# Optimization experiments

Hardware: AMD Instinct MI355X
Metric: run time of the kernel (lower is better)

Reference implementation:

```python
import jax, jax.numpy as jnp
import numpy as np

ALPHA = 0.1  # config['alpha']


def setup_inputs() -> dict:
    key = jax.random.key(0)
    k1, k2, k3, k4, k5 = jax.random.split(key, 5)
    n_bs, bit, n_cls, class_bit, n_train = 128, 48, 100, 16, 10000
    u = jax.random.normal(k1, (n_bs, bit), dtype=jnp.float32)
    # multi-hot labels (float, as in torch: y.float())
    y = jax.random.bernoulli(k2, 0.1, (n_bs, n_cls)).astype(jnp.float32)
    ind = jnp.arange(n_bs, dtype=jnp.int64)  # distinct in-range row indices
    # buffers mid-training: U holds previous class-wise codes, Y previous labels
    U = jax.random.normal(k3, (n_train, n_cls, class_bit), dtype=jnp.float32) * 0.1
    Y = jax.random.bernoulli(k4, 0.1, (n_train, n_cls)).astype(jnp.float32)
    # xavier_uniform-like init for w_D [n_class, bit, class_bit]
    limit = np.sqrt(6.0 / (bit + class_bit)).astype(np.float32)
    w_D = jax.random.uniform(k5, (n_cls, bit, class_bit), dtype=jnp.float32,
                             minval=-limit, maxval=limit)
    return {"u": u, "y": y, "ind": ind, "U": U, "Y": Y, "w_D": w_D}


def reference(u, y, ind, U, Y, w_D):
    # update label buffer: self.Y[ind, :] = y
    Y = Y.at[ind].set(y)
    # u_ = matmul(u, w_D).permute(1,0,2): [n_bs, n_cls, class_bit]
    u_ = jnp.einsum('bk,ckd->bcd', u, w_D)
    # update code buffer with detached u_ (torch: self.U[ind] = u_.data)
    U = U.at[ind].set(jax.lax.stop_gradient(u_))
    # pairwise similarity s: [n_bs, n_train, n_cls]
    s = y[:, None, :] * Y[None, :, :]
    # inner_product: sum over class_bit -> [n_bs, n_train, n_cls]
    ip = jnp.einsum('tcd,bcd->btc', U, u_)
    # stable log(1 + exp(ip)) - s*ip, exactly as the torch expression
    likelihood = (jnp.log1p(jnp.exp(-jnp.abs(ip))) + jnp.maximum(ip, 0.0)
                  - s * ip).mean()
    quantization = ALPHA * jnp.mean((u_ - jnp.sign(u_)) ** 2)
    return likelihood + quantization
```

## Files before the change

kernel.cpp:

```cpp
#include <hip/hip_runtime.h>
#include <math.h>

#define CB 16
#define ALPHA 0.1f
#define LOG2E 1.4426950408889634f
#define LN2F  0.6931471805599453f
#define MAXW 8
#define N_BS 128
#define BIT  48
#define UPAD 52

typedef __bf16 bf16x8 __attribute__((ext_vector_type(8)));
typedef float  f32x16 __attribute__((ext_vector_type(16)));

__global__ __launch_bounds__(256, 4) void loss_fused(
        const float* __restrict__ u, const float* __restrict__ y,
        const float* __restrict__ w_D,
        const float* __restrict__ U, const float* __restrict__ Yb,
        const int* __restrict__ ind,
        float* __restrict__ partials, float* __restrict__ quant_partials,
        int n_cls, int n_train, int ntile, int GY) {
    __shared__ float smf[N_BS * UPAD + 4 * BIT * CB];
    __shared__ int pflag[MAXW * 32];
    float* u_lds   = smf;
    float* wd_lds  = smf + N_BS * UPAD;
    float* u_slice = smf;

    const int tid  = threadIdx.x;
    const int lane = tid & 63;
    const int wid  = tid >> 6;
    const int bx   = blockIdx.x;
    const int by   = blockIdx.y;
    const int c    = bx * 4 + wid;
    const int r    = lane & 31;
    const int h    = lane >> 5;
    const int nw   = (ntile - by + GY - 1) / GY;

    pflag[tid] = -1;
    #pragma unroll
    for (int it = 0; it < N_BS * (BIT / 4) / 256; ++it) {
        int f = it * 256 + tid;
        int b = f / (BIT / 4), k4 = f % (BIT / 4);
        *(float4*)&u_lds[b * UPAD + k4 * 4] =
            *(const float4*)&u[(size_t)b * BIT + k4 * 4];
    }
    #pragma unroll
    for (int it = 0; it < 4 * BIT * (CB / 4) / 256; ++it) {
        int f = it * 256 + tid;
        int cc = f / (BIT * CB / 4), rest = f % (BIT * CB / 4);
        *(float4*)&wd_lds[cc * BIT * CB + rest * 4] =
            *(const float4*)&w_D[(size_t)(bx * 4 + cc) * BIT * CB + rest * 4];
    }
    __syncthreads();

    if (tid < N_BS) {
        int t = ind[tid];
        for (int w = 0; w < nw; ++w) {
            unsigned rl = (unsigned)(t - (by + w * GY) * 32);
            if (rl < 32u) pflag[w * 32 + rl] = tid;
        }
    }

    float acc0[8] = {0,0,0,0,0,0,0,0};
    float acc1[8] = {0,0,0,0,0,0,0,0};
    float acc2[8] = {0,0,0,0,0,0,0,0};
    float acc3[8] = {0,0,0,0,0,0,0,0};
    {
        const float* __restrict__ wdc = wd_lds + wid * BIT * CB + h * 8;
        for (int k4 = 0; k4 < BIT / 4; ++k4) {
            float4 ub0 = *(const float4*)&u_lds[(0 * 32 + r) * UPAD + k4 * 4];
            float4 ub1 = *(const float4*)&u_lds[(1 * 32 + r) * UPAD + k4 * 4];
            float4 ub2 = *(const float4*)&u_lds[(2 * 32 + r) * UPAD + k4 * 4];
            float4 ub3 = *(const float4*)&u_lds[(3 * 32 + r) * UPAD + k4 * 4];
            #pragma unroll
            for (int kk = 0; kk < 4; ++kk) {
                const float* wrow = wdc + (k4 * 4 + kk) * CB;
                float w8[8];
                float4 wa = *(const float4*)(wrow);
                float4 wb = *(const float4*)(wrow + 4);
                w8[0]=wa.x; w8[1]=wa.y; w8[2]=wa.z; w8[3]=wa.w;
                w8[4]=wb.x; w8[5]=wb.y; w8[6]=wb.z; w8[7]=wb.w;
                float s0 = (&ub0.x)[kk], s1 = (&ub1.x)[kk];
                float s2 = (&ub2.x)[kk], s3 = (&ub3.x)[kk];
                #pragma unroll
                for (int j = 0; j < 8; ++j) {
                    acc0[j] = fmaf(s0, w8[j], acc0[j]);
                    acc1[j] = fmaf(s1, w8[j], acc1[j]);
                    acc2[j] = fmaf(s2, w8[j], acc2[j]);
                    acc3[j] = fmaf(s3, w8[j], acc3[j]);
                }
            }
        }
    }

    if (by == 0) {
        float q = 0.f;
        #pragma unroll
        for (int j = 0; j < 8; ++j) {
            float v, sgn, d;
            v = acc0[j]; sgn = (v>0.f)?1.f:((v<0.f)?-1.f:0.f); d = v-sgn; q = fmaf(d,d,q);
            v = acc1[j]; sgn = (v>0.f)?1.f:((v<0.f)?-1.f:0.f); d = v-sgn; q = fmaf(d,d,q);
            v = acc2[j]; sgn = (v>0.f)?1.f:((v<0.f)?-1.f:0.f); d = v-sgn; q = fmaf(d,d,q);
            v = acc3[j]; sgn = (v>0.f)?1.f:((v<0.f)?-1.f:0.f); d = v-sgn; q = fmaf(d,d,q);
        }
        #pragma unroll
        for (int off = 32; off > 0; off >>= 1) q += __shfl_down(q, off, 64);
        if (lane == 0) quant_partials[bx * 4 + wid] = q;
    }

    float ypc0 = y[(size_t)(0 * 32 + r) * n_cls + c];
    float ypc1 = y[(size_t)(1 * 32 + r) * n_cls + c];
    float ypc2 = y[(size_t)(2 * 32 + r) * n_cls + c];
    float ypc3 = y[(size_t)(3 * 32 + r) * n_cls + c];
    float vv[8], ww[8];
    #pragma unroll
    for (int j = 0; j < 8; ++j) {
        ww[j] = acc0[j] + acc1[j] + acc2[j] + acc3[j];
        vv[j] = ypc0*acc0[j] + ypc1*acc1[j] + ypc2*acc2[j] + ypc3*acc3[j];
    }
    #pragma unroll
    for (int m = 1; m < 32; m <<= 1) {
        #pragma unroll
        for (int j = 0; j < 8; ++j) {
            vv[j] += __shfl_xor(vv[j], m, 64);
            ww[j] += __shfl_xor(ww[j], m, 64);
        }
    }

    bf16x8 B0, B1, B2, B3;
    #pragma unroll
    for (int j = 0; j < 8; ++j) {
        B0[j] = (__bf16)(acc0[j] * LOG2E);
        B1[j] = (__bf16)(acc1[j] * LOG2E);
        B2[j] = (__bf16)(acc2[j] * LOG2E);
        B3[j] = (__bf16)(acc3[j] * LOG2E);
    }

    __syncthreads();
    {
        float* dst = u_slice + wid * N_BS * CB + r * CB + h * 8;
        *(float4*)(dst + 0*32*CB)     = make_float4(acc0[0],acc0[1],acc0[2],acc0[3]);
        *(float4*)(dst + 0*32*CB + 4) = make_float4(acc0[4],acc0[5],acc0[6],acc0[7]);
        *(float4*)(dst + 1*32*CB)     = make_float4(acc1[0],acc1[1],acc1[2],acc1[3]);
        *(float4*)(dst + 1*32*CB + 4) = make_float4(acc1[4],acc1[5],acc1[6],acc1[7]);
        *(float4*)(dst + 2*32*CB)     = make_float4(acc2[0],acc2[1],acc2[2],acc2[3]);
        *(float4*)(dst + 2*32*CB + 4) = make_float4(acc2[4],acc2[5],acc2[6],acc2[7]);
        *(float4*)(dst + 3*32*CB)     = make_float4(acc3[0],acc3[1],acc3[2],acc3[3]);
        *(float4*)(dst + 3*32*CB + 4) = make_float4(acc3[4],acc3[5],acc3[6],acc3[7]);
    }
    __syncthreads();

    float acc = 0.f;
    f32x16 zc = {};
    #pragma unroll 1
    for (int w = 0; w < nw; ++w) {
        const int t0  = (by + w * GY) * 32;
        const int row = t0 + r;
        const int rc  = (row < n_train) ? row : (n_train - 1);
        const float* __restrict__ ar = U + ((size_t)rc * n_cls + c) * CB + h * 8;
        float4 a0 = *(const float4*)(ar);
        float4 a1 = *(const float4*)(ar + 4);
        float Yv = Yb[(size_t)rc * n_cls + c];

        const int pf = pflag[w * 32 + r];
        if (pf >= 0) {
            const float* src = u_slice + wid * N_BS * CB + pf * CB + h * 8;
            a0 = *(const float4*)(src);
            a1 = *(const float4*)(src + 4);
            Yv = y[(size_t)pf * n_cls + c];
        }
        if (row >= n_train) {
            a0 = make_float4(0.f, 0.f, 0.f, 0.f); a1 = a0; Yv = 0.f;
        }

        float sv = a0.x*vv[0] + a0.y*vv[1] + a0.z*vv[2] + a0.w*vv[3]
                 + a1.x*vv[4] + a1.y*vv[5] + a1.z*vv[6] + a1.w*vv[7];
        float sw = a0.x*ww[0] + a0.y*ww[1] + a0.z*ww[2] + a0.w*ww[3]
                 + a1.x*ww[4] + a1.y*ww[5] + a1.z*ww[6] + a1.w*ww[7];

        bf16x8 A;
        A[0] = (__bf16)a0.x; A[1] = (__bf16)a0.y;
        A[2] = (__bf16)a0.z; A[3] = (__bf16)a0.w;
        A[4] = (__bf16)a1.x; A[5] = (__bf16)a1.y;
        A[6] = (__bf16)a1.z; A[7] = (__bf16)a1.w;

        float accA = 0.f;
        float pp   = 1.f;
        #pragma unroll
        for (int bt = 0; bt < 4; ++bt) {
            bf16x8 Bf = (bt == 0) ? B0 : (bt == 1) ? B1 : (bt == 2) ? B2 : B3;
            f32x16 D = __builtin_amdgcn_mfma_f32_32x32x16_bf16(A, Bf, zc,
                                                               0, 0, 0);
            float a[16];
            #pragma unroll
            for (int j = 0; j < 16; ++j) {
                float ipa = fabsf(D[j]);
                a[j] = 1.0f + __builtin_amdgcn_exp2f(-ipa);
                accA += ipa;
            }
            #pragma unroll
            for (int s = 1; s < 16; s <<= 1)
                #pragma unroll
                for (int j = 0; j < 16; j += 2 * s) a[j] *= a[j + s];
            pp *= a[0];
        }
        float accL = __builtin_amdgcn_logf(pp);
        acc += LN2F * accL + (0.5f * LN2F) * accA + 0.5f * sw - Yv * sv;
    }

    #pragma unroll
    for (int off = 32; off > 0; off >>= 1)
        acc += __shfl_down(acc, off, 64);
    if (lane == 0) {
        int bid = by * gridDim.x + bx;
        partials[bid * 4 + wid] = acc;
    }
}

__global__ __launch_bounds__(256) void finalize_kernel(
        const float* __restrict__ partials, int nblk,
        const float* __restrict__ quant_partials, int n_quant,
        float* __restrict__ out, double pad_corr,
        double like_scale, double quant_scale) {
    double s = 0.0, q = 0.0;
    for (int i = threadIdx.x; i < nblk; i += 256) s += (double)partials[i];
    for (int i = threadIdx.x; i < n_quant; i += 256) q += (double)quant_partials[i];
    #pragma unroll
    for (int off = 32; off > 0; off >>= 1) {
        s += __shfl_down(s, off, 64);
        q += __shfl_down(q, off, 64);
    }
    __shared__ double dred[4][2];
    int lane = threadIdx.x & 63, wid = threadIdx.x >> 6;
    if (lane == 0) { dred[wid][0] = s; dred[wid][1] = q; }
    __syncthreads();
    if (threadIdx.x == 0) {
        double S = dred[0][0] + dred[1][0] + dred[2][0] + dred[3][0];
        double Q = dred[0][1] + dred[1][1] + dred[2][1] + dred[3][1];
        out[0] = (float)((S - pad_corr) * like_scale + Q * quant_scale);
    }
}

extern "C" void kernel_launch(void* const* d_in, const int* in_sizes, int n_in,
                              void* d_out, int out_size, void* d_ws, size_t ws_size,
                              hipStream_t stream) {
    const float* u   = (const float*)d_in[0];
    const float* y   = (const float*)d_in[1];
    const int*   ind = (const int*)d_in[2];
    const float* U   = (const float*)d_in[3];
    const float* Yb  = (const float*)d_in[4];
    const float* w_D = (const float*)d_in[5];

    const int n_bs    = in_sizes[2];
    const int n_cls   = in_sizes[1] / n_bs;
    const int n_train = in_sizes[4] / n_cls;

    const int totalU = n_bs * n_cls * CB;
    const int ntile  = (n_train + 31) / 32;
    const int GY     = (ntile + MAXW - 1) / MAXW;
    const int gx     = (n_cls + 3) / 4;
    const int nblk   = GY * gx;
    const int npart  = nblk * 4;
    const int nquant = gx * 4;

    char* ws = (char*)d_ws;
    size_t off = 0;
    float* partials = (float*)(ws + off);        off += (size_t)npart * 4;
    float* quant_partials = (float*)(ws + off);  off += (size_t)nquant * 4;

    loss_fused<<<dim3(gx, GY), 256, 0, stream>>>(
        u, y, w_D, U, Yb, ind, partials, quant_partials,
        n_cls, n_train, ntile, GY);

    const double ln2 = 0.6931471805599453;
    const double n_pad = (double)((long long)(ntile * 32 - n_train) *
                                  (long long)n_bs * (long long)n_cls);
    const double pad_corr    = ln2 * n_pad;
    const double like_scale  = 1.0 / ((double)n_bs * n_train * n_cls);
    const double quant_scale = (double)ALPHA / (double)totalU;

    finalize_kernel<<<1, 256, 0, stream>>>(partials, npart,
                                           quant_partials, nquant,
                                           (float*)d_out, pad_corr,
                                           like_scale, quant_scale);
}
```

Before: 49.41 us.

## Drop LDS staging of u and w_D, store u_ slice as packed bf16

The kernel no longer copies u and w_D into shared memory before the small projection matmul. Each lane now reads its operands straight from global memory, relying on caches. The per-wave u_ slice used to patch overwritten buffer rows is stored as packed bf16 pairs in a much smaller LDS array, which also removes one block-wide barrier. This lowers LDS footprint and prologue staging cost, which may help occupancy. In exchange, the prologue does strided, uncoalesced global loads, and the patched rows now enter the fp32 sv/sw dot products at bf16 precision.

New measurement: 58.49 us. +18.4%, slower.

```diff
diff --git a/kernel.cpp b/kernel.cpp
--- a/kernel.cpp
+++ b/kernel.cpp
@@ -8,10 +8,14 @@
 #define MAXW 8
 #define N_BS 128
 #define BIT  48
-#define UPAD 52
 
 typedef __bf16 bf16x8 __attribute__((ext_vector_type(8)));
 typedef float  f32x16 __attribute__((ext_vector_type(16)));
+
+__device__ __forceinline__ unsigned int f2bf(float x) {
+    unsigned int v = __float_as_uint(x);
+    return (v + 0x7FFFu + ((v >> 16) & 1u)) >> 16;
+}
 
 __global__ __launch_bounds__(256, 4) void loss_fused(
         const float* __restrict__ u, const float* __restrict__ y,
@@ -20,11 +24,8 @@
         const int* __restrict__ ind,
         float* __restrict__ partials, float* __restrict__ quant_partials,
         int n_cls, int n_train, int ntile, int GY) {
-    __shared__ float smf[N_BS * UPAD + 4 * BIT * CB];
+    __shared__ unsigned int ubf32[4 * N_BS * 9];
     __shared__ int pflag[MAXW * 32];
-    float* u_lds   = smf;
-    float* wd_lds  = smf + N_BS * UPAD;
-    float* u_slice = smf;
 
     const int tid  = threadIdx.x;
     const int lane = tid & 63;
@@ -37,22 +38,7 @@
     const int nw   = (ntile - by + GY - 1) / GY;
 
     pflag[tid] = -1;
-    #pragma unroll
-    for (int it = 0; it < N_BS * (BIT / 4) / 256; ++it) {
-        int f = it * 256 + tid;
-        int b = f / (BIT / 4), k4 = f % (BIT / 4);
-        *(float4*)&u_lds[b * UPAD + k4 * 4] =
-            *(const float4*)&u[(size_t)b * BIT + k4 * 4];
-    }
-    #pragma unroll
-    for (int it = 0; it < 4 * BIT * (CB / 4) / 256; ++it) {
-        int f = it * 256 + tid;
-        int cc = f / (BIT * CB / 4), rest = f % (BIT * CB / 4);
-        *(float4*)&wd_lds[cc * BIT * CB + rest * 4] =
-            *(const float4*)&w_D[(size_t)(bx * 4 + cc) * BIT * CB + rest * 4];
-    }
     __syncthreads();
-
     if (tid < N_BS) {
         int t = ind[tid];
         for (int w = 0; w < nw; ++w) {
@@ -66,18 +52,22 @@
     float acc2[8] = {0,0,0,0,0,0,0,0};
     float acc3[8] = {0,0,0,0,0,0,0,0};
     {
-        const float* __restrict__ wdc = wd_lds + wid * BIT * CB + h * 8;
+        const float* __restrict__ wdc = w_D + (size_t)c * BIT * CB + h * 8;
+        const float* __restrict__ ub0p = u + (size_t)(0 * 32 + r) * BIT;
+        const float* __restrict__ ub1p = u + (size_t)(1 * 32 + r) * BIT;
+        const float* __restrict__ ub2p = u + (size_t)(2 * 32 + r) * BIT;
+        const float* __restrict__ ub3p = u + (size_t)(3 * 32 + r) * BIT;
         for (int k4 = 0; k4 < BIT / 4; ++k4) {
-            float4 ub0 = *(const float4*)&u_lds[(0 * 32 + r) * UPAD + k4 * 4];
-            float4 ub1 = *(const float4*)&u_lds[(1 * 32 + r) * UPAD + k4 * 4];
-            float4 ub2 = *(const float4*)&u_lds[(2 * 32 + r) * UPAD + k4 * 4];
-            float4 ub3 = *(const float4*)&u_lds[(3 * 32 + r) * UPAD + k4 * 4];
+            float4 ub0 = *(const float4*)(ub0p + k4 * 4);
+            float4 ub1 = *(const float4*)(ub1p + k4 * 4);
+            float4 ub2 = *(const float4*)(ub2p + k4 * 4);
+            float4 ub3 = *(const float4*)(ub3p + k4 * 4);
             #pragma unroll
             for (int kk = 0; kk < 4; ++kk) {
                 const float* wrow = wdc + (k4 * 4 + kk) * CB;
-                float w8[8];
                 float4 wa = *(const float4*)(wrow);
                 float4 wb = *(const float4*)(wrow + 4);
+                float w8[8];
                 w8[0]=wa.x; w8[1]=wa.y; w8[2]=wa.z; w8[3]=wa.w;
                 w8[4]=wb.x; w8[5]=wb.y; w8[6]=wb.z; w8[7]=wb.w;
                 float s0 = (&ub0.x)[kk], s1 = (&ub1.x)[kk];
@@ -127,6 +117,20 @@
         }
     }
 
+    {
+        unsigned int* d0 = &ubf32[(wid * N_BS + 0 * 32 + r) * 9 + h * 4];
+        unsigned int* d1 = &ubf32[(wid * N_BS + 1 * 32 + r) * 9 + h * 4];
+        unsigned int* d2 = &ubf32[(wid * N_BS + 2 * 32 + r) * 9 + h * 4];
+        unsigned int* d3 = &ubf32[(wid * N_BS + 3 * 32 + r) * 9 + h * 4];
+        #pragma unroll
+        for (int j2 = 0; j2 < 4; ++j2) {
+            d0[j2] = f2bf(acc0[2*j2]) | (f2bf(acc0[2*j2+1]) << 16);
+            d1[j2] = f2bf(acc1[2*j2]) | (f2bf(acc1[2*j2+1]) << 16);
+            d2[j2] = f2bf(acc2[2*j2]) | (f2bf(acc2[2*j2+1]) << 16);
+            d3[j2] = f2bf(acc3[2*j2]) | (f2bf(acc3[2*j2+1]) << 16);
+        }
+    }
+
     bf16x8 B0, B1, B2, B3;
     #pragma unroll
     for (int j = 0; j < 8; ++j) {
@@ -136,18 +140,6 @@
         B3[j] = (__bf16)(acc3[j] * LOG2E);
     }
 
-    __syncthreads();
-    {
-        float* dst = u_slice + wid * N_BS * CB + r * CB + h * 8;
-        *(float4*)(dst + 0*32*CB)     = make_float4(acc0[0],acc0[1],acc0[2],acc0[3]);
-        *(float4*)(dst + 0*32*CB + 4) = make_float4(acc0[4],acc0[5],acc0[6],acc0[7]);
-        *(float4*)(dst + 1*32*CB)     = make_float4(acc1[0],acc1[1],acc1[2],acc1[3]);
-        *(float4*)(dst + 1*32*CB + 4) = make_float4(acc1[4],acc1[5],acc1[6],acc1[7]);
-        *(float4*)(dst + 2*32*CB)     = make_float4(acc2[0],acc2[1],acc2[2],acc2[3]);
-        *(float4*)(dst + 2*32*CB + 4) = make_float4(acc2[4],acc2[5],acc2[6],acc2[7]);
-        *(float4*)(dst + 3*32*CB)     = make_float4(acc3[0],acc3[1],acc3[2],acc3[3]);
-        *(float4*)(dst + 3*32*CB + 4) = make_float4(acc3[4],acc3[5],acc3[6],acc3[7]);
-    }
     __syncthreads();
 
     float acc = 0.f;
@@ -164,9 +156,16 @@
 
         const int pf = pflag[w * 32 + r];
         if (pf >= 0) {
-            const float* src = u_slice + wid * N_BS * CB + pf * CB + h * 8;
-            a0 = *(const float4*)(src);
-            a1 = *(const float4*)(src + 4);
+            const unsigned int* src = &ubf32[(wid * N_BS + pf) * 9 + h * 4];
+            unsigned int w0 = src[0], w1 = src[1], w2 = src[2], w3 = src[3];
+            a0.x = __uint_as_float(w0 << 16);
+            a0.y = __uint_as_float(w0 & 0xFFFF0000u);
+            a0.z = __uint_as_float(w1 << 16);
+            a0.w = __uint_as_float(w1 & 0xFFFF0000u);
+            a1.x = __uint_as_float(w2 << 16);
+            a1.y = __uint_as_float(w2 & 0xFFFF0000u);
+            a1.z = __uint_as_float(w3 << 16);
+            a1.w = __uint_as_float(w3 & 0xFFFF0000u);
             Yv = y[(size_t)pf * n_cls + c];
         }
         if (row >= n_train) {
```
